# Kernel tuning notes

Measured on AMD Instinct MI355X. Metric: run time of the kernel, lower is better.

The kernel has to match this reference:

```python
import jax, jax.numpy as jnp
import numpy as np
import math

N_NODES, CHANNELS, N_ELEM, N_FEAT = 4096, 128, 10, 128
LS_IN = [0, 1, 2]          # input irreps per channel: 0e+1o+2e -> dim 9
L_OUT = [0, 1]             # keep_irrep_out = {0e, 1o}
L12_MAX = 3                # cap on intermediate coupling
SLICES = {0: (0, 1), 1: (1, 4), 2: (4, 9)}
PATHS1 = [l for l in L_OUT if l in LS_IN]
PATHS2 = [(l1, l2, lo) for l1 in LS_IN for l2 in LS_IN for lo in L_OUT if abs(l1 - l2) <= lo <= l1 + l2]
T12_KEYS = [(l1, l2, l12) for l1 in LS_IN for l2 in LS_IN for l12 in range(abs(l1 - l2), min(l1 + l2, L12_MAX) + 1)]
PATHS3 = [(k, l3, lo) for k in T12_KEYS for l3 in LS_IN for lo in L_OUT if abs(k[2] - l3) <= lo <= k[2] + l3]

def _su2_cg(j1, m1, j2, m2, j3, m3):
    if m3 != m1 + m2:
        return 0.0
    f = math.factorial
    vmin = max(-j1 + j2 + m3, -j1 + m1, 0)
    vmax = min(j2 + j3 + m1, j3 - j1 + j2, j3 + m3)
    C = math.sqrt((2 * j3 + 1) * f(j3 + j1 - j2) * f(j3 - j1 + j2) * f(j1 + j2 - j3) * f(j3 + m3) * f(j3 - m3)
                  / (f(j1 + j2 + j3 + 1) * f(j1 - m1) * f(j1 + m1) * f(j2 - m2) * f(j2 + m2)))
    S = 0.0
    for v in range(vmin, vmax + 1):
        S += (-1) ** (v + j2 + m2) * f(j2 + j3 + m1 - v) * f(j1 - m1 + v) / (
            f(v) * f(j3 - j1 + j2 - v) * f(j3 + m3 - v) * f(v + j1 - j2 - m3))
    return C * S

def _c2r(l):
    # change of basis real -> complex spherical harmonics (e3nn convention)
    q = np.zeros((2 * l + 1, 2 * l + 1), dtype=np.complex128)
    for m in range(-l, 0):
        q[l + m, l + abs(m)] = 1.0 / math.sqrt(2)
        q[l + m, l - abs(m)] = -1j / math.sqrt(2)
    q[l, l] = 1.0
    for m in range(1, l + 1):
        q[l + m, l + abs(m)] = (-1) ** m / math.sqrt(2)
        q[l + m, l - abs(m)] = 1j * (-1) ** m / math.sqrt(2)
    return (-1j) ** l * q

_CG = {}
def real_cg(l1, l2, l3):
    key = (l1, l2, l3)
    if key not in _CG:
        Cc = np.zeros((2 * l1 + 1, 2 * l2 + 1, 2 * l3 + 1), dtype=np.complex128)
        for i, m1 in enumerate(range(-l1, l1 + 1)):
            for j, m2 in enumerate(range(-l2, l2 + 1)):
                for k, m3 in enumerate(range(-l3, l3 + 1)):
                    Cc[i, j, k] = _su2_cg(l1, m1, l2, m2, l3, m3)
        R = np.einsum('ij,kl,mn,ikn->jlm', _c2r(l1), _c2r(l2), np.conj(_c2r(l3).T), Cc)
        _CG[key] = np.real(R).astype(np.float32)
    return _CG[key]

def setup_inputs():
    key = jax.random.key(0)
    k = jax.random.split(key, 8)
    node_feats = jax.random.normal(k[0], (N_NODES, CHANNELS, 9), dtype=jnp.float32)
    species = jax.random.randint(k[1], (N_NODES,), 0, N_ELEM)
    w1 = jax.random.normal(k[2], (N_ELEM, len(PATHS1), CHANNELS), dtype=jnp.float32) / math.sqrt(len(PATHS1))
    w2 = jax.random.normal(k[3], (N_ELEM, len(PATHS2), CHANNELS), dtype=jnp.float32) / math.sqrt(len(PATHS2))
    w3 = jax.random.normal(k[4], (N_ELEM, len(PATHS3), CHANNELS), dtype=jnp.float32) / math.sqrt(len(PATHS3))
    lin_w0 = jax.random.normal(k[5], (CHANNELS, N_FEAT), dtype=jnp.float32)
    lin_w1 = jax.random.normal(k[6], (CHANNELS, N_FEAT), dtype=jnp.float32)
    return {"node_feats": node_feats, "w1": w1, "w2": w2, "w3": w3,
            "lin_w0": lin_w0, "lin_w1": lin_w1, "species": species}

def reference(node_feats, w1, w2, w3, lin_w0, lin_w1, species):
    n, c = node_feats.shape[:2]
    attrs = jax.nn.one_hot(species, N_ELEM, dtype=node_feats.dtype)
    A = {l: node_feats[..., SLICES[l][0]:SLICES[l][1]] for l in LS_IN}
    # element-dependent path weights per node
    w1n = jnp.einsum('ne,epc->npc', attrs, w1)
    w2n = jnp.einsum('ne,epc->npc', attrs, w2)
    w3n = jnp.einsum('ne,epc->npc', attrs, w3)
    B = {lo: jnp.zeros((n, c, 2 * lo + 1), node_feats.dtype) for lo in L_OUT}
    # correlation order 1
    for p, lo in enumerate(PATHS1):
        B[lo] = B[lo] + w1n[:, p, :, None] * A[lo]
    for p, (l1, l2, lo) in enumerate(PATHS2):
        cg = jnp.asarray(real_cg(l1, l2, lo))
        t = jnp.einsum('ijk,nci,ncj->nck', cg, A[l1], A[l2])
        B[lo] = B[lo] + w2n[:, p, :, None] * t
    T12 = {}
    for kk in T12_KEYS:
        l1, l2, l12 = kk
        T12[kk] = jnp.einsum('ijk,nci,ncj->nck', jnp.asarray(real_cg(l1, l2, l12)), A[l1], A[l2])
    for p, (kk, l3, lo) in enumerate(PATHS3):
        cg = jnp.asarray(real_cg(kk[2], l3, lo))
        t = jnp.einsum('ijk,nci,ncj->nck', cg, T12[kk], A[l3])
        B[lo] = B[lo] + w3n[:, p, :, None] * t
    # equivariant Linear: mix channel axis into num_features per output irrep
    s = 1.0 / math.sqrt(c)
    out0 = jnp.einsum('ncm,cf->nfm', B[0], lin_w0) * s
    out1 = jnp.einsum('ncm,cf->nfm', B[1], lin_w1) * s
    return jnp.concatenate([out0, out1], axis=-1)  # [N, F, 1+3]
```

## Files before the change

kernel.cpp:

```cpp
#include <hip/hip_runtime.h>
#include <utility>


#define NN 4096
#define NC 128
#define NE 10

typedef float v2f __attribute__((ext_vector_type(2)));

__device__ __forceinline__ v2f ld2(const float* p) {
  return *reinterpret_cast<const v2f*>(p);
}
__device__ __forceinline__ v2f cfma(float c, v2f x, v2f a) {
  v2f cc = {c, c};
  return __builtin_elementwise_fma(cc, x, a);
}
__device__ __forceinline__ v2f vfma(v2f w, v2f x, v2f a) {
  return __builtin_elementwise_fma(w, x, a);
}

template<typename F, int... Is>
__device__ __forceinline__ void sfor_impl(F&& f, std::integer_sequence<int, Is...>) {
  (f(std::integral_constant<int, Is>{}), ...);
}
template<int N, typename F>
__device__ __forceinline__ void sfor(F&& f) {
  sfor_impl((F&&)f, std::make_integer_sequence<int, N>{});
}

constexpr int T_L1c[19]  = {0,0,0,1,1,1,1,1,1,1,2,2,2,2,2,2,2,2,3};
constexpr int T_L2c[19]  = {0,1,2,0,1,1,1,2,2,2,0,1,1,1,2,2,2,2,2};
constexpr int T_L3c[19]  = {0,1,2,1,0,1,2,1,2,3,2,1,2,3,0,1,2,3,1};
constexpr int T_OFFc[19] = {0,1,10,35,44,53,80,125,170,245,350,375,420,495,600,625,700,825,1000};
constexpr int AOFFc[3]   = {0,1,4};

constexpr int P2U_L1c[7]  = {0,0,1,1,1,2,2};
constexpr int P2U_L2c[7]  = {0,1,1,1,2,2,2};
constexpr int P2U_LOc[7]  = {0,1,0,1,1,0,1};
constexpr int P2U_TBLc[7] = {0,1,4,5,7,14,15};
constexpr int P2U_WAc[7]  = {0,1,3,4,5,7,8};
constexpr int P2U_WBc[7]  = {-1,2,-1,-1,6,-1,-1};

constexpr int K_L1c[18]  = {0,0,0,1,1,1,1,1,1,1,2,2,2,2,2,2,2,2};
constexpr int K_L2c[18]  = {0,1,2,0,1,1,1,2,2,2,0,1,1,1,2,2,2,2};
constexpr int K_L12c[18] = {0,1,2,1,0,1,2,1,2,3,2,1,2,3,0,1,2,3};

constexpr int   TT_CANONc[18] = {0,1,2,1,4,5,6,7,8,9,2,7,8,9,14,15,16,17};
constexpr float TT_SGNc[18]   = {1,1,1,1,1,1,1,1,1,1,1,1,-1,1,1,1,1,1};
constexpr int CANONc[13] = {0,1,2,4,5,6,7,8,9,14,15,16,17};
constexpr int CONS2c[13] = {-1,3,10,-1,-1,-1,11,12,13,-1,-1,-1,-1};

constexpr int P3_STARTc[19] = {0,2,6,9,13,15,19,22,26,29,30,33,37,40,41,43,47,50,51};
constexpr int P3_L3c[51] = {
  0,1,  0,1,1,2,  1,2,2,  0,1,1,2,  0,1,  0,1,1,2,  1,2,2,  0,1,1,2,  1,2,2,
  2,  1,2,2,  0,1,1,2,  1,2,2,  2,  0,1,  0,1,1,2,  1,2,2,  2 };
constexpr int P3_LOc[51] = {
  0,1,  1,0,1,1,  1,0,1,  1,0,1,1,  0,1,  1,0,1,1,  1,0,1,  1,0,1,1,  1,0,1,
  1,  1,0,1,  1,0,1,1,  1,0,1,  1,  0,1,  1,0,1,1,  1,0,1,  1 };
constexpr int P3_TBLc[51] = {
  0,1,  3,4,5,7,  11,14,15,  3,4,5,7,  0,1,  3,4,5,7,  11,14,15,  3,4,5,7,
  11,14,15,  18,  11,14,15,  3,4,5,7,  11,14,15,  18,  0,1,  3,4,5,7,
  11,14,15,  18 };

constexpr double cfact(int n) { double r = 1.0; for (int i = 2; i <= n; ++i) r *= i; return r; }
constexpr double csqrt(double x) {
  if (x <= 0.0) return 0.0;
  double r = x > 1.0 ? x : 1.0;
  for (int i = 0; i < 64; ++i) r = 0.5 * (r + x / r);
  return r;
}
constexpr double su2cg(int j1, int m1, int j2, int m2, int j3, int m3) {
  if (m3 != m1 + m2) return 0.0;
  int vmin = -j1 + j2 + m3; if (-j1 + m1 > vmin) vmin = -j1 + m1; if (vmin < 0) vmin = 0;
  int vmax = j2 + j3 + m1; if (j3 - j1 + j2 < vmax) vmax = j3 - j1 + j2; if (j3 + m3 < vmax) vmax = j3 + m3;
  double C = csqrt((2.0 * j3 + 1.0)
                   * cfact(j3 + j1 - j2) * cfact(j3 - j1 + j2) * cfact(j1 + j2 - j3)
                   * cfact(j3 + m3) * cfact(j3 - m3)
                   / (cfact(j1 + j2 + j3 + 1) * cfact(j1 - m1) * cfact(j1 + m1)
                      * cfact(j2 - m2) * cfact(j2 + m2)));
  double S = 0.0;
  for (int v = vmin; v <= vmax; ++v) {
    double sgn = ((v + j2 + m2) & 1) ? -1.0 : 1.0;
    S += sgn * cfact(j2 + j3 + m1 - v) * cfact(j1 - m1 + v)
         / (cfact(v) * cfact(j3 - j1 + j2 - v) * cfact(j3 + m3 - v) * cfact(v + j1 - j2 - m3));
  }
  return C * S;
}

struct Cx { double re, im; };
constexpr Cx cxmul(Cx a, Cx b) { return Cx{a.re * b.re - a.im * b.im, a.re * b.im + a.im * b.re}; }
struct Row { int cnt; int col[2]; Cx v[2]; };

constexpr Row c2r_row(int l, int r) {
  Row out{0, {0, 0}, {{0, 0}, {0, 0}}};
  constexpr double is2 = 0.70710678118654752440;
  const int m = r - l;
  if (m < 0) {
    out.cnt = 2;
    out.col[0] = l - m; out.v[0] = Cx{is2, 0.0};
    out.col[1] = l + m; out.v[1] = Cx{0.0, -is2};
  } else if (m == 0) {
    out.cnt = 1; out.col[0] = l; out.v[0] = Cx{1.0, 0.0};
  } else {
    const double sgn = (m & 1) ? -1.0 : 1.0;
    out.cnt = 2;
    out.col[0] = l + m; out.v[0] = Cx{sgn * is2, 0.0};
    out.col[1] = l - m; out.v[1] = Cx{0.0, sgn * is2};
  }
  const int ph = l & 3;
  for (int a = 0; a < out.cnt; ++a) {
    Cx v = out.v[a];
    out.v[a] = (ph == 0) ? v
             : (ph == 1) ? Cx{v.im, -v.re}
             : (ph == 2) ? Cx{-v.re, -v.im}
                         : Cx{-v.im, v.re};
  }
  return out;
}

struct CGAll { float v[1105]; };
constexpr CGAll make_cg() {
  CGAll R{};
  for (int t = 0; t < 19; ++t) {
    const int l1 = T_L1c[t], l2 = T_L2c[t], l3 = T_L3c[t], off = T_OFFc[t];
    const int d1 = 2 * l1 + 1, d2 = 2 * l2 + 1, d3 = 2 * l3 + 1;
    double tmp[175] = {};
    for (int i = 0; i < d1; ++i) {
      const int m1 = i - l1;
      const Row r1 = c2r_row(l1, i);
      for (int k = 0; k < d2; ++k) {
        const int m2 = k - l2, m3 = m1 + m2;
        if (m3 < -l3 || m3 > l3) continue;
        const double cc = su2cg(l1, m1, l2, m2, l3, m3);
        if (cc == 0.0) continue;
        const Row r2 = c2r_row(l2, k);
        const Row r3 = c2r_row(l3, m3 + l3);
        for (int a = 0; a < r1.cnt; ++a)
          for (int b = 0; b < r2.cnt; ++b) {
            const Cx q12 = cxmul(r1.v[a], r2.v[b]);
            for (int cdx = 0; cdx < r3.cnt; ++cdx) {
              const double re = q12.re * r3.v[cdx].re + q12.im * r3.v[cdx].im;
              tmp[(r1.col[a] * d2 + r2.col[b]) * d3 + r3.col[cdx]] += re * cc;
            }
          }
      }
    }
    const int sz = d1 * d2 * d3;
    for (int e = 0; e < sz; ++e) R.v[off + e] = (float)tmp[e];
  }
  return R;
}
constexpr CGAll CG_ALL = make_cg();

constexpr bool check_cg_sym() {
  for (int t = 0; t < 18; ++t) {
    const int tc = TT_CANONc[t];
    if (tc == t) continue;
    const int l1 = K_L1c[t], l2 = K_L2c[t], l12 = K_L12c[t];
    const int d1 = 2*l1+1, d2 = 2*l2+1, d12 = 2*l12+1;
    for (int i = 0; i < d1; ++i)
      for (int j = 0; j < d2; ++j)
        for (int k = 0; k < d12; ++k) {
          float a = CG_ALL.v[T_OFFc[t]  + (i*d2 + j)*d12 + k];
          float b = TT_SGNc[t] * CG_ALL.v[T_OFFc[tc] + (j*d1 + i)*d12 + k];
          float d = a - b; if (d < 0) d = -d;
          if (d > 1e-5f) return false;
        }
  }
  return true;
}
static_assert(check_cg_sym(), "CG exchange symmetry violated");

__global__ __launch_bounds__(256, 3) void epb_fused(
    const float*  __restrict__ nf,
    const float*  __restrict__ w1,
    const float*  __restrict__ w2,
    const float*  __restrict__ w3,
    const float4* __restrict__ lw0_4,
    const float4* __restrict__ lw1_4,
    const int*    __restrict__ species,
    float* __restrict__ out)
{
  __shared__ float4 Bsh[4 * NC];
  __shared__ float4 Red[16 * NC];

  const int t  = threadIdx.x;
  const int nb = blockIdx.x * 4;

  {
    const int nl = t >> 6;
    const int c0 = (t & 63) * 2;
    const int n  = nb + nl;
    const int s  = species[n];

    const float* ap = nf + ((size_t)n * NC + c0) * 9;
    v2f A[9];
    sfor<9>([&](auto I) { A[I.value] = v2f{ap[I.value], ap[I.value + 9]}; });

    const float* w1p = w1 + (size_t)s * 2  * NC + c0;
    const float* w2p = w2 + (size_t)s * 9  * NC + c0;
    const float* w3p = w3 + (size_t)s * 51 * NC + c0;

    v2f B[4];
    {
      const v2f wa = ld2(w1p), wb = ld2(w1p + NC);
      B[0] = wa * A[0];
      B[1] = wb * A[1];
      B[2] = wb * A[2];
      B[3] = wb * A[3];
    }

    sfor<7>([&](auto P) {
      constexpr int p  = P.value;
      constexpr int l1 = P2U_L1c[p], l2 = P2U_L2c[p], lo = P2U_LOc[p];
      constexpr int d1 = 2*l1+1, d2 = 2*l2+1, dl = 2*lo+1;
      constexpr int off = T_OFFc[P2U_TBLc[p]];
      v2f w = ld2(w2p + P2U_WAc[p] * NC);
      if constexpr (P2U_WBc[p] >= 0) w = w + ld2(w2p + P2U_WBc[p] * NC);
      sfor<dl>([&](auto Kk) {
        constexpr int k = Kk.value;
        v2f v = {0.f, 0.f};
        sfor<d1>([&](auto I) {
          sfor<d2>([&](auto J) {
            constexpr float cgc = CG_ALL.v[off + (I.value * d2 + J.value) * dl + k];
            if constexpr (cgc != 0.0f) {
              constexpr int ia = AOFFc[l1] + I.value, ja = AOFFc[l2] + J.value;
              constexpr int x = ia < ja ? ia : ja, y = ia < ja ? ja : ia;
              v = cfma(cgc, A[x] * A[y], v);
            }
          });
        });
        B[lo + k] = vfma(w, v, B[lo + k]);
      });
    });

    sfor<13>([&](auto CI) {
      constexpr int tk  = CANONc[CI.value];
      constexpr int l1  = K_L1c[tk], l2 = K_L2c[tk], l12 = K_L12c[tk];
      constexpr int d1  = 2*l1+1, d2 = 2*l2+1, d12 = 2*l12+1;
      constexpr int off = T_OFFc[tk];
      v2f tt[d12];
      sfor<d12>([&](auto Kk) {
        constexpr int k = Kk.value;
        v2f v = {0.f, 0.f};
        sfor<d1>([&](auto I) {
          sfor<d2>([&](auto J) {
            constexpr float cgc = CG_ALL.v[off + (I.value * d2 + J.value) * d12 + k];
            if constexpr (cgc != 0.0f) {
              constexpr int ia = AOFFc[l1] + I.value, ja = AOFFc[l2] + J.value;
              constexpr int x = ia < ja ? ia : ja, y = ia < ja ? ja : ia;
              v = cfma(cgc, A[x] * A[y], v);
            }
          });
        });
        tt[k] = v;
      });

      auto consume = [&](auto TK, auto SG) {
        constexpr int tkey = TK.value;
        constexpr float sgn = (float)SG.value;
        constexpr int pcnt = P3_STARTc[tkey + 1] - P3_STARTc[tkey];
        sfor<pcnt>([&](auto PP) {
          constexpr int p  = P3_STARTc[tkey] + PP.value;
          constexpr int l3 = P3_L3c[p], lo = P3_LOc[p];
          constexpr int d3 = 2*l3+1, dl = 2*lo+1;
          constexpr int off2 = T_OFFc[P3_TBLc[p]];
          const v2f w = ld2(w3p + p * NC);
          sfor<dl>([&](auto M) {
            v2f v = {0.f, 0.f};
            sfor<d12>([&](auto Kk) {
              sfor<d3>([&](auto J) {
                constexpr float cgc = sgn * CG_ALL.v[off2 + (Kk.value * d3 + J.value) * dl + M.value];
                if constexpr (cgc != 0.0f)
                  v = cfma(cgc, tt[Kk.value] * A[AOFFc[l3] + J.value], v);
              });
            });
            B[lo + M.value] = vfma(w, v, B[lo + M.value]);
          });
        });
      };
      consume(std::integral_constant<int, tk>{}, std::integral_constant<int, 1>{});
      constexpr int td = CONS2c[CI.value];
      if constexpr (td >= 0)
        consume(std::integral_constant<int, td>{},
                std::integral_constant<int, (int)TT_SGNc[td]>{});
    });

    Bsh[nl * NC + c0]     = make_float4(B[0].x, B[1].x, B[2].x, B[3].x);
    Bsh[nl * NC + c0 + 1] = make_float4(B[0].y, B[1].y, B[2].y, B[3].y);
  }
  __syncthreads();

  const int q   = t & 31;
  const int dup = (t >> 5) & 1;
  const int wv  = t >> 6;
  const int n0  = dup * 2;

  float4 acc[2][4] = {};

  const float4* w0c = lw0_4 + (size_t)(wv * 32) * 32 + q;
  const float4* w1c = lw1_4 + (size_t)(wv * 32) * 32 + q;
  const float4* bp0 = &Bsh[ n0      * NC + wv * 32];
  const float4* bp1 = &Bsh[(n0 + 1) * NC + wv * 32];

  #pragma unroll 2
  for (int i = 0; i < 32; ++i) {
    const float4 wa = w0c[i * 32];
    const float4 wb = w1c[i * 32];
    const float4 ba = bp0[i];
    const float4 bb = bp1[i];
#define FQ(f, waf, wbf) \
    acc[0][f].x = fmaf(ba.x, waf, acc[0][f].x); \
    acc[0][f].y = fmaf(ba.y, wbf, acc[0][f].y); \
    acc[0][f].z = fmaf(ba.z, wbf, acc[0][f].z); \
    acc[0][f].w = fmaf(ba.w, wbf, acc[0][f].w); \
    acc[1][f].x = fmaf(bb.x, waf, acc[1][f].x); \
    acc[1][f].y = fmaf(bb.y, wbf, acc[1][f].y); \
    acc[1][f].z = fmaf(bb.z, wbf, acc[1][f].z); \
    acc[1][f].w = fmaf(bb.w, wbf, acc[1][f].w);
    FQ(0, wa.x, wb.x)
    FQ(1, wa.y, wb.y)
    FQ(2, wa.z, wb.z)
    FQ(3, wa.w, wb.w)
#undef FQ
  }

  sfor<2>([&](auto NN_) {
    sfor<4>([&](auto F_) {
      Red[((n0 + NN_.value) * 4 + F_.value) * NC + wv * 32 + q] = acc[NN_.value][F_.value];
    });
  });
  __syncthreads();

  const float s4 = 0.08838834764831845f;
  float4* o4 = reinterpret_cast<float4*>(out);
  sfor<2>([&](auto O_) {
    const int oid = 2 * t + O_.value;
    const int n   = oid >> 7;
    const int rem = oid & 127;
    const int row = (n * 4 + (rem & 3)) * NC + (rem >> 2);
    const float4 r0 = Red[row];
    const float4 r1 = Red[row + 32];
    const float4 r2 = Red[row + 64];
    const float4 r3 = Red[row + 96];
    o4[(size_t)(nb + n) * NC + rem] = make_float4(
        ((r0.x + r1.x) + (r2.x + r3.x)) * s4,
        ((r0.y + r1.y) + (r2.y + r3.y)) * s4,
        ((r0.z + r1.z) + (r2.z + r3.z)) * s4,
        ((r0.w + r1.w) + (r2.w + r3.w)) * s4);
  });
}

extern "C" void kernel_launch(void* const* d_in, const int* in_sizes, int n_in,
                              void* d_out, int out_size, void* d_ws, size_t ws_size,
                              hipStream_t stream) {
  const float* nf  = (const float*)d_in[0];
  const float* w1  = (const float*)d_in[1];
  const float* w2  = (const float*)d_in[2];
  const float* w3  = (const float*)d_in[3];
  const float* lw0 = (const float*)d_in[4];
  const float* lw1 = (const float*)d_in[5];
  const int*   spc = (const int*)  d_in[6];
  float* out = (float*)d_out;
  (void)d_ws; (void)ws_size; (void)in_sizes; (void)n_in; (void)out_size;

  hipLaunchKernelGGL(epb_fused, dim3(NN / 4), dim3(256), 0, stream,
                     nf, w1, w2, w3, (const float4*)lw0, (const float4*)lw1,
                     spc, out);
}
```

Before: 110.8 us.

## Process one channel per thread with scalar math and two nodes per block

Each thread now handles a single channel instead of a pair, dropping the packed two-wide float math for scalar FMAs. Blocks cover two nodes instead of four, which halves shared memory and doubles the grid. The launch-bounds occupancy hint rises from 3 to 8, so the compiler must fit fewer registers per thread. The linear stage now gives each thread one node, so every lin_w load feeds half as many FMAs. Risks are losing the packed-FMA throughput, register spills under the tighter bound, and more global traffic for lin_w per output.

```diff
diff --git a/kernel.cpp b/kernel.cpp
--- a/kernel.cpp
+++ b/kernel.cpp
@@ -6,18 +6,7 @@
 #define NC 128
 #define NE 10
 
-typedef float v2f __attribute__((ext_vector_type(2)));
-
-__device__ __forceinline__ v2f ld2(const float* p) {
-  return *reinterpret_cast<const v2f*>(p);
-}
-__device__ __forceinline__ v2f cfma(float c, v2f x, v2f a) {
-  v2f cc = {c, c};
-  return __builtin_elementwise_fma(cc, x, a);
-}
-__device__ __forceinline__ v2f vfma(v2f w, v2f x, v2f a) {
-  return __builtin_elementwise_fma(w, x, a);
-}
+typedef float f4u __attribute__((ext_vector_type(4), aligned(4)));
 
 template<typename F, int... Is>
 __device__ __forceinline__ void sfor_impl(F&& f, std::integer_sequence<int, Is...>) {
@@ -171,7 +160,7 @@
 }
 static_assert(check_cg_sym(), "CG exchange symmetry violated");
 
-__global__ __launch_bounds__(256, 3) void epb_fused(
+__global__ __launch_bounds__(256, 8) void epb_fused(
     const float*  __restrict__ nf,
     const float*  __restrict__ w1,
     const float*  __restrict__ w2,
@@ -181,29 +170,34 @@
     const int*    __restrict__ species,
     float* __restrict__ out)
 {
-  __shared__ float4 Bsh[4 * NC];
-  __shared__ float4 Red[16 * NC];
+  __shared__ float4 Bsh[2 * NC];
+  __shared__ float4 Red[8 * NC];
 
   const int t  = threadIdx.x;
-  const int nb = blockIdx.x * 4;
+  const int nb = blockIdx.x * 2;
 
   {
-    const int nl = t >> 6;
-    const int c0 = (t & 63) * 2;
+    const int nl = t >> 7;
+    const int c  = t & 127;
     const int n  = nb + nl;
     const int s  = species[n];
 
-    const float* ap = nf + ((size_t)n * NC + c0) * 9;
-    v2f A[9];
-    sfor<9>([&](auto I) { A[I.value] = v2f{ap[I.value], ap[I.value + 9]}; });
-
-    const float* w1p = w1 + (size_t)s * 2  * NC + c0;
-    const float* w2p = w2 + (size_t)s * 9  * NC + c0;
-    const float* w3p = w3 + (size_t)s * 51 * NC + c0;
-
-    v2f B[4];
+    const float* ap = nf + ((size_t)n * NC + c) * 9;
+    float A[9];
     {
-      const v2f wa = ld2(w1p), wb = ld2(w1p + NC);
+      const f4u v0 = *reinterpret_cast<const f4u*>(ap);
+      const f4u v1 = *reinterpret_cast<const f4u*>(ap + 4);
+      sfor<4>([&](auto I) { A[I.value] = v0[I.value]; A[I.value + 4] = v1[I.value]; });
+      A[8] = ap[8];
+    }
+
+    const float* w1p = w1 + (size_t)s * 2  * NC + c;
+    const float* w2p = w2 + (size_t)s * 9  * NC + c;
+    const float* w3p = w3 + (size_t)s * 51 * NC + c;
+
+    float B[4];
+    {
+      const float wa = w1p[0], wb = w1p[NC];
       B[0] = wa * A[0];
       B[1] = wb * A[1];
       B[2] = wb * A[2];
@@ -215,22 +209,22 @@
       constexpr int l1 = P2U_L1c[p], l2 = P2U_L2c[p], lo = P2U_LOc[p];
       constexpr int d1 = 2*l1+1, d2 = 2*l2+1, dl = 2*lo+1;
       constexpr int off = T_OFFc[P2U_TBLc[p]];
-      v2f w = ld2(w2p + P2U_WAc[p] * NC);
-      if constexpr (P2U_WBc[p] >= 0) w = w + ld2(w2p + P2U_WBc[p] * NC);
+      float w = w2p[P2U_WAc[p] * NC];
+      if constexpr (P2U_WBc[p] >= 0) w += w2p[P2U_WBc[p] * NC];
       sfor<dl>([&](auto Kk) {
         constexpr int k = Kk.value;
-        v2f v = {0.f, 0.f};
+        float v = 0.f;
         sfor<d1>([&](auto I) {
           sfor<d2>([&](auto J) {
             constexpr float cgc = CG_ALL.v[off + (I.value * d2 + J.value) * dl + k];
             if constexpr (cgc != 0.0f) {
               constexpr int ia = AOFFc[l1] + I.value, ja = AOFFc[l2] + J.value;
               constexpr int x = ia < ja ? ia : ja, y = ia < ja ? ja : ia;
-              v = cfma(cgc, A[x] * A[y], v);
+              v = fmaf(cgc, A[x] * A[y], v);
             }
           });
         });
-        B[lo + k] = vfma(w, v, B[lo + k]);
+        B[lo + k] = fmaf(w, v, B[lo + k]);
       });
     });
 
@@ -239,17 +233,17 @@
       constexpr int l1  = K_L1c[tk], l2 = K_L2c[tk], l12 = K_L12c[tk];
       constexpr int d1  = 2*l1+1, d2 = 2*l2+1, d12 = 2*l12+1;
       constexpr int off = T_OFFc[tk];
-      v2f tt[d12];
+      float tt[d12];
       sfor<d12>([&](auto Kk) {
         constexpr int k = Kk.value;
-        v2f v = {0.f, 0.f};
+        float v = 0.f;
         sfor<d1>([&](auto I) {
           sfor<d2>([&](auto J) {
             constexpr float cgc = CG_ALL.v[off + (I.value * d2 + J.value) * d12 + k];
             if constexpr (cgc != 0.0f) {
               constexpr int ia = AOFFc[l1] + I.value, ja = AOFFc[l2] + J.value;
               constexpr int x = ia < ja ? ia : ja, y = ia < ja ? ja : ia;
-              v = cfma(cgc, A[x] * A[y], v);
+              v = fmaf(cgc, A[x] * A[y], v);
             }
           });
         });
@@ -265,17 +259,17 @@
           constexpr int l3 = P3_L3c[p], lo = P3_LOc[p];
           constexpr int d3 = 2*l3+1, dl = 2*lo+1;
           constexpr int off2 = T_OFFc[P3_TBLc[p]];
-          const v2f w = ld2(w3p + p * NC);
+          const float w = w3p[p * NC];
           sfor<dl>([&](auto M) {
-            v2f v = {0.f, 0.f};
+            float v = 0.f;
             sfor<d12>([&](auto Kk) {
               sfor<d3>([&](auto J) {
                 constexpr float cgc = sgn * CG_ALL.v[off2 + (Kk.value * d3 + J.value) * dl + M.value];
                 if constexpr (cgc != 0.0f)
-                  v = cfma(cgc, tt[Kk.value] * A[AOFFc[l3] + J.value], v);
+                  v = fmaf(cgc, tt[Kk.value] * A[AOFFc[l3] + J.value], v);
               });
             });
-            B[lo + M.value] = vfma(w, v, B[lo + M.value]);
+            B[lo + M.value] = fmaf(w, v, B[lo + M.value]);
           });
         });
       };
@@ -286,58 +280,45 @@
                 std::integral_constant<int, (int)TT_SGNc[td]>{});
     });
 
-    Bsh[nl * NC + c0]     = make_float4(B[0].x, B[1].x, B[2].x, B[3].x);
-    Bsh[nl * NC + c0 + 1] = make_float4(B[0].y, B[1].y, B[2].y, B[3].y);
+    Bsh[nl * NC + c] = make_float4(B[0], B[1], B[2], B[3]);
   }
   __syncthreads();
 
   const int q   = t & 31;
-  const int dup = (t >> 5) & 1;
-  const int wv  = t >> 6;
-  const int n0  = dup * 2;
-
-  float4 acc[2][4] = {};
+  const int wv  = (t >> 5) & 3;
+  const int nl2 = t >> 7;
+
+  float4 acc[4] = {};
 
   const float4* w0c = lw0_4 + (size_t)(wv * 32) * 32 + q;
   const float4* w1c = lw1_4 + (size_t)(wv * 32) * 32 + q;
-  const float4* bp0 = &Bsh[ n0      * NC + wv * 32];
-  const float4* bp1 = &Bsh[(n0 + 1) * NC + wv * 32];
-
-  #pragma unroll 2
+  const float4* bp  = &Bsh[nl2 * NC + wv * 32];
+
+  #pragma unroll 4
   for (int i = 0; i < 32; ++i) {
     const float4 wa = w0c[i * 32];
     const float4 wb = w1c[i * 32];
-    const float4 ba = bp0[i];
-    const float4 bb = bp1[i];
-#define FQ(f, waf, wbf) \
-    acc[0][f].x = fmaf(ba.x, waf, acc[0][f].x); \
-    acc[0][f].y = fmaf(ba.y, wbf, acc[0][f].y); \
-    acc[0][f].z = fmaf(ba.z, wbf, acc[0][f].z); \
-    acc[0][f].w = fmaf(ba.w, wbf, acc[0][f].w); \
-    acc[1][f].x = fmaf(bb.x, waf, acc[1][f].x); \
-    acc[1][f].y = fmaf(bb.y, wbf, acc[1][f].y); \
-    acc[1][f].z = fmaf(bb.z, wbf, acc[1][f].z); \
-    acc[1][f].w = fmaf(bb.w, wbf, acc[1][f].w);
-    FQ(0, wa.x, wb.x)
-    FQ(1, wa.y, wb.y)
-    FQ(2, wa.z, wb.z)
-    FQ(3, wa.w, wb.w)
-#undef FQ
-  }
-
-  sfor<2>([&](auto NN_) {
-    sfor<4>([&](auto F_) {
-      Red[((n0 + NN_.value) * 4 + F_.value) * NC + wv * 32 + q] = acc[NN_.value][F_.value];
-    });
+    const float4 b  = bp[i];
+    acc[0].x = fmaf(b.x, wa.x, acc[0].x); acc[0].y = fmaf(b.y, wb.x, acc[0].y);
+    acc[0].z = fmaf(b.z, wb.x, acc[0].z); acc[0].w = fmaf(b.w, wb.x, acc[0].w);
+    acc[1].x = fmaf(b.x, wa.y, acc[1].x); acc[1].y = fmaf(b.y, wb.y, acc[1].y);
+    acc[1].z = fmaf(b.z, wb.y, acc[1].z); acc[1].w = fmaf(b.w, wb.y, acc[1].w);
+    acc[2].x = fmaf(b.x, wa.z, acc[2].x); acc[2].y = fmaf(b.y, wb.z, acc[2].y);
+    acc[2].z = fmaf(b.z, wb.z, acc[2].z); acc[2].w = fmaf(b.w, wb.z, acc[2].w);
+    acc[3].x = fmaf(b.x, wa.w, acc[3].x); acc[3].y = fmaf(b.y, wb.w, acc[3].y);
+    acc[3].z = fmaf(b.z, wb.w, acc[3].z); acc[3].w = fmaf(b.w, wb.w, acc[3].w);
+  }
+
+  sfor<4>([&](auto F_) {
+    Red[(nl2 * 4 + F_.value) * NC + wv * 32 + q] = acc[F_.value];
   });
   __syncthreads();
 
   const float s4 = 0.08838834764831845f;
   float4* o4 = reinterpret_cast<float4*>(out);
-  sfor<2>([&](auto O_) {
-    const int oid = 2 * t + O_.value;
-    const int n   = oid >> 7;
-    const int rem = oid & 127;
+  {
+    const int n   = t >> 7;
+    const int rem = t & 127;
     const int row = (n * 4 + (rem & 3)) * NC + (rem >> 2);
     const float4 r0 = Red[row];
     const float4 r1 = Red[row + 32];
@@ -348,7 +329,7 @@
         ((r0.y + r1.y) + (r2.y + r3.y)) * s4,
         ((r0.z + r1.z) + (r2.z + r3.z)) * s4,
         ((r0.w + r1.w) + (r2.w + r3.w)) * s4);
-  });
+  }
 }
 
 extern "C" void kernel_launch(void* const* d_in, const int* in_sizes, int n_in,
@@ -364,7 +345,7 @@
   float* out = (float*)d_out;
   (void)d_ws; (void)ws_size; (void)in_sizes; (void)n_in; (void)out_size;
 
-  hipLaunchKernelGGL(epb_fused, dim3(NN / 4), dim3(256), 0, stream,
+  hipLaunchKernelGGL(epb_fused, dim3(NN / 2), dim3(256), 0, stream,
                      nf, w1, w2, w3, (const float4*)lw0, (const float4*)lw1,
                      spc, out);
 }
```

After: 245.4 us. 121% more time.
